# Kernel optimization log

Measured on AMD Instinct MI355X. Metric: run time of the kernel, lower is better.

Reference implementation:

```python
import jax, jax.numpy as jnp
import numpy as np

APPERTURE = 256
Q_SCALE = 0.06


def setup_inputs() -> dict:
    key = jax.random.key(0)
    ks = jax.random.split(key, 5)
    B, N, D_IN, D_OUT = 4, 4096, 1024, 1024
    std = 1.0 / np.sqrt(D_IN)
    x = jax.random.normal(ks[0], (B, N, D_IN), dtype=jnp.float32)
    Wk = jax.random.normal(ks[1], (D_OUT, D_IN), dtype=jnp.float32) * std
    Wq = jax.random.normal(ks[2], (D_OUT, D_IN), dtype=jnp.float32) * std
    Wv = jax.random.normal(ks[3], (D_OUT, D_IN), dtype=jnp.float32) * std
    Wo = jax.random.normal(ks[4], (D_IN, D_OUT), dtype=jnp.float32) * std
    return {"x": x, "Wk": Wk, "Wq": Wq, "Wv": Wv, "Wo": Wo}


def reference(x, Wk, Wq, Wv, Wo):
    # x: [B, N, D_in]; torch Linear(W) computes x @ W.T
    K = jnp.einsum('bnd,od->bno', x, Wk)          # [B, N, D_out]
    Q = jnp.einsum('bnd,od->bno', x, Wq) * Q_SCALE
    V = jnp.einsum('bnd,od->bno', x, Wv)
    logits = jnp.einsum('bno,bmo->bnm', Q, K)      # [B, N, N]
    N = x.shape[1]
    idx = jnp.arange(N)
    # tril(-a) + triu(a) masks |i-j| >= apperture (keep strict band)
    band_mask = jnp.abs(idx[:, None] - idx[None, :]) >= APPERTURE  # [N, N]
    logits = jnp.where(band_mask[None, :, :], -jnp.inf, logits)
    att_weights = jax.nn.softmax(logits, axis=-1)  # [B, N, N]
    # dropout is identity in eval mode
    # y = (V^T @ weights)^T  ->  y[b,n,:] = sum_m att[b,m,n] * V[b,m,:]
    y = jnp.einsum('bmn,bmo->bno', att_weights, V)
    y = jnp.einsum('bno,io->bni', y, Wo)           # [B, N, D_in]
    return (y, att_weights)
```

## Files before the change

### kernel.cpp

```cpp
#include <hip/hip_runtime.h>
#include <stdint.h>

#define SEQ 4096
#define DM  1024
#define NB  4
#define QSCALE 0.06f

typedef __attribute__((ext_vector_type(8))) short short8;
typedef __attribute__((ext_vector_type(4))) float floatx4;

__device__ __forceinline__ unsigned short f2bf(float f) {
  union { float f; unsigned int u; } v; v.f = f;
  unsigned int u = v.u;
  u += 0x7FFFu + ((u >> 16) & 1u);
  return (unsigned short)(u >> 16);
}

__device__ __forceinline__ void async16(const void* g, void* l) {
  __builtin_amdgcn_global_load_lds(
      (const __attribute__((address_space(1))) void*)g,
      (__attribute__((address_space(3))) void*)l, 16, 0, 0);
}

__global__ void cvt_all(const float* __restrict__ x, const float* __restrict__ wk,
                        const float* __restrict__ wq, const float* __restrict__ wv,
                        const float* __restrict__ wo, unsigned short* __restrict__ xb,
                        unsigned short* __restrict__ wb) {
  int blk = blockIdx.x;
  const float* src;
  unsigned short* dst;
  int i;
  if (blk < 8192) {
    src = x; dst = xb; i = (blk * 256 + threadIdx.x) * 8;
  } else {
    int w = blk - 8192;
    int sel = w >> 9;
    src = sel == 0 ? wk : sel == 1 ? wq : sel == 2 ? wv : wo;
    dst = wb + sel * 1048576;
    i = ((w & 511) * 256 + threadIdx.x) * 8;
  }
  const float4* p = (const float4*)(src + i);
  float4 a = p[0], b = p[1];
  short8 o;
  o[0] = (short)f2bf(a.x); o[1] = (short)f2bf(a.y);
  o[2] = (short)f2bf(a.z); o[3] = (short)f2bf(a.w);
  o[4] = (short)f2bf(b.x); o[5] = (short)f2bf(b.y);
  o[6] = (short)f2bf(b.z); o[7] = (short)f2bf(b.w);
  *(short8*)(dst + i) = o;
}

template <bool OUT_BF16, int MT, int NT, bool DUAL>
__global__ __launch_bounds__(512, 2) void gemm256(
    const unsigned short* __restrict__ A, const unsigned short* __restrict__ W,
    void* __restrict__ C0, void* __restrict__ C1, float a0, float a1, long ldc) {
  __shared__ __align__(16) unsigned short lds[4 * 16384];
  const int K = 1024;
  const int NKT = 32;
  int tid = threadIdx.x;
  int lane = tid & 63;
  int wid = tid >> 6;
  int wr = wid >> 2, wc = wid & 3;

  const int CPX = (MT * NT) >> 3;
  int bid = blockIdx.x;
  int raw = (bid & 7) * CPX + (bid >> 3);
  int bx = raw % MT;
  int by = raw / MT;
  long brow = (long)bx * 256;
  long bcol = (long)by * 256;

  floatx4 acc[8][4];
#pragma unroll
  for (int i = 0; i < 8; i++)
#pragma unroll
    for (int j = 0; j < 4; j++) acc[i][j] = (floatx4){0.f, 0.f, 0.f, 0.f};

  const unsigned short* Ag = A + (brow + (tid >> 2)) * K + (tid & 3) * 8;
  const unsigned short* Wg = W + (bcol + (tid >> 2)) * K + (tid & 3) * 8;
  unsigned short* ldsW = lds + wid * 512;

  int aRd = (wr * 128 + (lane & 15)) * 32 + (lane >> 4) * 8;
  int bRd = (wc * 64 + (lane & 15)) * 32 + (lane >> 4) * 8;

#pragma unroll
  for (int tt = 0; tt < 3; tt++) {
    unsigned short* d = ldsW + tt * 16384;
    const unsigned short* a = Ag + tt * 32;
    const unsigned short* w = Wg + tt * 32;
    async16(a, d);
    async16(a + 128 * K, d + 4096);
    async16(w, d + 8192);
    async16(w + 128 * K, d + 12288);
  }
  asm volatile("s_waitcnt vmcnt(8)" ::: "memory");
  __builtin_amdgcn_s_barrier();

  for (int t = 0; t < NKT; ++t) {
    const unsigned short* bufA = lds + (t & 3) * 16384;
    const unsigned short* bufB = bufA + 8192;
    short8 a0f[4], b0f[4], a1f[4];
#pragma unroll
    for (int mt = 0; mt < 4; mt++)
      a0f[mt] = *(const short8*)(bufA + aRd + mt * 512);
#pragma unroll
    for (int nt = 0; nt < 4; nt++)
      b0f[nt] = *(const short8*)(bufB + bRd + nt * 512);
    if (t + 3 < NKT) {
      unsigned short* d = ldsW + ((t + 3) & 3) * 16384;
      const unsigned short* a = Ag + (t + 3) * 32;
      async16(a, d);
      async16(a + 128 * K, d + 4096);
    }
    __builtin_amdgcn_s_barrier();
    __builtin_amdgcn_s_setprio(1);
#pragma unroll
    for (int mt = 0; mt < 4; mt++)
#pragma unroll
      for (int nt = 0; nt < 4; nt++)
        acc[mt][nt] = __builtin_amdgcn_mfma_f32_16x16x32_bf16(
            a0f[mt], b0f[nt], acc[mt][nt], 0, 0, 0);
    __builtin_amdgcn_s_setprio(0);
    __builtin_amdgcn_s_barrier();
#pragma unroll
    for (int mt = 0; mt < 4; mt++)
      a1f[mt] = *(const short8*)(bufA + aRd + 2048 + mt * 512);
    if (t + 3 < NKT) {
      unsigned short* d = ldsW + ((t + 3) & 3) * 16384;
      const unsigned short* w = Wg + (t + 3) * 32;
      async16(w, d + 8192);
      async16(w + 128 * K, d + 12288);
    }
    __builtin_amdgcn_s_barrier();
    __builtin_amdgcn_s_setprio(1);
#pragma unroll
    for (int mt = 0; mt < 4; mt++)
#pragma unroll
      for (int nt = 0; nt < 4; nt++)
        acc[4 + mt][nt] = __builtin_amdgcn_mfma_f32_16x16x32_bf16(
            a1f[mt], b0f[nt], acc[4 + mt][nt], 0, 0, 0);
    __builtin_amdgcn_s_setprio(0);
    if (t < NKT - 3)
      asm volatile("s_waitcnt vmcnt(8)" ::: "memory");
    else if (t == NKT - 3)
      asm volatile("s_waitcnt vmcnt(4)" ::: "memory");
    else
      asm volatile("s_waitcnt vmcnt(0)" ::: "memory");
    __builtin_amdgcn_s_barrier();
  }

  void* Cp;
  float alpha;
  long cc;
  if (DUAL && by >= NT / 2) {
    Cp = C1; alpha = a1; cc = bcol - (long)(NT / 2) * 256;
  } else {
    Cp = C0; alpha = a0; cc = bcol;
  }
  long crow = brow + wr * 128 + (lane >> 4) * 4;
  long ccol = cc + wc * 64 + (lane & 15);
#pragma unroll
  for (int mt = 0; mt < 8; mt++)
#pragma unroll
    for (int nt = 0; nt < 4; nt++)
#pragma unroll
      for (int r = 0; r < 4; r++) {
        float v = acc[mt][nt][r] * alpha;
        long idx = (crow + mt * 16 + r) * ldc + ccol + nt * 16;
        if (OUT_BF16)
          ((unsigned short*)Cp)[idx] = f2bf(v);
        else
          ((float*)Cp)[idx] = v;
      }
}

__global__ __launch_bounds__(512, 2) void logits256(
    const unsigned short* __restrict__ Qb, const unsigned short* __restrict__ Kb,
    float* __restrict__ att) {
  int b = blockIdx.z;
  int n0 = blockIdx.x * 256;
  int m0 = n0 + ((int)blockIdx.y - 1) * 256;
  if (m0 < 0 || m0 >= SEQ) return;
  __shared__ __align__(16) unsigned short lds[4 * 16384];
  const int K = 1024;
  const int NKT = 32;
  int tid = threadIdx.x;
  int lane = tid & 63;
  int wid = tid >> 6;
  int wr = wid >> 2, wc = wid & 3;

  floatx4 acc[8][4];
#pragma unroll
  for (int i = 0; i < 8; i++)
#pragma unroll
    for (int j = 0; j < 4; j++) acc[i][j] = (floatx4){0.f, 0.f, 0.f, 0.f};

  const unsigned short* Ag =
      Qb + ((long)b * SEQ + n0 + (tid >> 2)) * K + (tid & 3) * 8;
  const unsigned short* Wg =
      Kb + ((long)b * SEQ + m0 + (tid >> 2)) * K + (tid & 3) * 8;
  unsigned short* ldsW = lds + wid * 512;

  int aRd = (wr * 128 + (lane & 15)) * 32 + (lane >> 4) * 8;
  int bRd = (wc * 64 + (lane & 15)) * 32 + (lane >> 4) * 8;

#pragma unroll
  for (int tt = 0; tt < 3; tt++) {
    unsigned short* d = ldsW + tt * 16384;
    const unsigned short* a = Ag + tt * 32;
    const unsigned short* w = Wg + tt * 32;
    async16(a, d);
    async16(a + 128 * K, d + 4096);
    async16(w, d + 8192);
    async16(w + 128 * K, d + 12288);
  }
  asm volatile("s_waitcnt vmcnt(8)" ::: "memory");
  __builtin_amdgcn_s_barrier();

  for (int t = 0; t < NKT; ++t) {
    const unsigned short* bufA = lds + (t & 3) * 16384;
    const unsigned short* bufB = bufA + 8192;
    short8 a0f[4], b0f[4], a1f[4];
#pragma unroll
    for (int mt = 0; mt < 4; mt++)
      a0f[mt] = *(const short8*)(bufA + aRd + mt * 512);
#pragma unroll
    for (int nt = 0; nt < 4; nt++)
      b0f[nt] = *(const short8*)(bufB + bRd + nt * 512);
    if (t + 3 < NKT) {
      unsigned short* d = ldsW + ((t + 3) & 3) * 16384;
      const unsigned short* a = Ag + (t + 3) * 32;
      async16(a, d);
      async16(a + 128 * K, d + 4096);
    }
    __builtin_amdgcn_s_barrier();
    __builtin_amdgcn_s_setprio(1);
#pragma unroll
    for (int mt = 0; mt < 4; mt++)
#pragma unroll
      for (int nt = 0; nt < 4; nt++)
        acc[mt][nt] = __builtin_amdgcn_mfma_f32_16x16x32_bf16(
            a0f[mt], b0f[nt], acc[mt][nt], 0, 0, 0);
    __builtin_amdgcn_s_setprio(0);
    __builtin_amdgcn_s_barrier();
#pragma unroll
    for (int mt = 0; mt < 4; mt++)
      a1f[mt] = *(const short8*)(bufA + aRd + 2048 + mt * 512);
    if (t + 3 < NKT) {
      unsigned short* d = ldsW + ((t + 3) & 3) * 16384;
      const unsigned short* w = Wg + (t + 3) * 32;
      async16(w, d + 8192);
      async16(w + 128 * K, d + 12288);
    }
    __builtin_amdgcn_s_barrier();
    __builtin_amdgcn_s_setprio(1);
#pragma unroll
    for (int mt = 0; mt < 4; mt++)
#pragma unroll
      for (int nt = 0; nt < 4; nt++)
        acc[4 + mt][nt] = __builtin_amdgcn_mfma_f32_16x16x32_bf16(
            a1f[mt], b0f[nt], acc[4 + mt][nt], 0, 0, 0);
    __builtin_amdgcn_s_setprio(0);
    if (t < NKT - 3)
      asm volatile("s_waitcnt vmcnt(8)" ::: "memory");
    else if (t == NKT - 3)
      asm volatile("s_waitcnt vmcnt(4)" ::: "memory");
    else
      asm volatile("s_waitcnt vmcnt(0)" ::: "memory");
    __builtin_amdgcn_s_barrier();
  }

  float* attB = att + (long)b * SEQ * SEQ;
  int crow = n0 + wr * 128 + (lane >> 4) * 4;
  int ccol = m0 + wc * 64 + (lane & 15);
#pragma unroll
  for (int mt = 0; mt < 8; mt++)
#pragma unroll
    for (int nt = 0; nt < 4; nt++)
#pragma unroll
      for (int r = 0; r < 4; r++) {
        int row = crow + mt * 16 + r;
        int col = ccol + nt * 16;
        int d = row - col;
        if (d < 256 && d > -256)
          attB[(long)row * SEQ + col] = acc[mt][nt][r];
      }
}

__global__ __launch_bounds__(256) void softmax_band(
    float* __restrict__ att, unsigned short* __restrict__ attT2) {
  __shared__ float e_lds[16 * 545];
  __shared__ float inv_s[16];
  int blk = blockIdx.x;
  int b = blk >> 8;
  int r0 = (blk & 255) * 16;
  int tid = threadIdx.x;
  int row = tid >> 4;
  int t16 = tid & 15;
  int i = r0 + row;
  int jbase = r0 - 272;
  float* arow = att + ((long)b * SEQ + i) * (long)SEQ;

  float raw[34];
  float m = -1e30f;
#pragma unroll
  for (int s = 0; s < 34; s++) {
    int jj = s * 16 + t16;
    int j = jbase + jj;
    bool ok = (j >= 0) && (j < SEQ) && (j >= i - 255) && (j <= i + 255);
    float v = ok ? arow[j] : -1e30f;
    raw[s] = v;
    m = fmaxf(m, v);
  }
#pragma unroll
  for (int off = 8; off; off >>= 1) m = fmaxf(m, __shfl_xor(m, off, 16));

  float sum = 0.f;
#pragma unroll
  for (int s = 0; s < 34; s++) {
    int jj = s * 16 + t16;
    float e = (raw[s] > -1e29f) ? __expf(raw[s] - m) : 0.f;
    e_lds[row * 545 + jj] = e;
    sum += e;
  }
#pragma unroll
  for (int off = 8; off; off >>= 1) sum += __shfl_xor(sum, off, 16);
  float invr = 1.0f / sum;
  if (t16 == 0) inv_s[row] = invr;
  __syncthreads();

  for (int s = 0; s < 64; s++) {
    int j0 = (s * 16 + t16) * 4;
    float4 w;
    float* wp = (float*)&w;
#pragma unroll
    for (int k = 0; k < 4; k++) {
      int j = j0 + k;
      bool ok = (j >= i - 255) && (j <= i + 255);
      int jj = j - jbase;
      jj = jj < 0 ? 0 : (jj > 543 ? 543 : jj);
      wp[k] = ok ? e_lds[row * 545 + jj] * invr : 0.f;
    }
    *(float4*)(arow + j0) = w;
  }

  int nn = tid >> 4;
  int mi16 = tid & 15;
  int i2 = r0 + mi16;
  float inv2 = inv_s[mi16];
  int Bc = r0 & ~255;
  for (int s = 0; s < 48; s++) {
    int n = Bc - 256 + s * 16 + nn;
    if (n < 0 || n >= SEQ) continue;
    int mi = i2 - (n & ~255) + 256;
    bool ok = (n >= i2 - 255) && (n <= i2 + 255);
    int jj = n - jbase;
    jj = jj < 0 ? 0 : (jj > 544 ? 544 : jj);
    float val = ok ? e_lds[mi16 * 545 + jj] * inv2 : 0.f;
    attT2[(((long)b * 16 + (n >> 8)) * 256 + (n & 255)) * 768 + mi] = f2bf(val);
  }
}

__global__ __launch_bounds__(512, 2) void attv256(
    const unsigned short* __restrict__ attT2, const unsigned short* __restrict__ Vt,
    unsigned short* __restrict__ yb) {
  __shared__ __align__(16) unsigned short lds[4 * 16384];
  const int KA = 768;
  const int NKT = 24;
  int b = blockIdx.z;
  int nb2 = blockIdx.x;
  int o0 = blockIdx.y * 256;
  int N0 = nb2 * 256;
  int tid = threadIdx.x;
  int lane = tid & 63;
  int wid = tid >> 6;
  int wr = wid >> 2, wc = wid & 3;

  floatx4 acc[8][4];
#pragma unroll
  for (int i = 0; i < 8; i++)
#pragma unroll
    for (int j = 0; j < 4; j++) acc[i][j] = (floatx4){0.f, 0.f, 0.f, 0.f};

  const unsigned short* Abase = attT2 + ((long)(b * 16 + nb2) * 256) * KA;
  const unsigned short* Ag = Abase + (long)(tid >> 2) * KA + (tid & 3) * 8;
  const unsigned short* Vg =
      Vt + (long)(o0 + (tid >> 2)) * (NB * SEQ) + (tid & 3) * 8;
  unsigned short* ldsW = lds + wid * 512;

  int aRd = (wr * 128 + (lane & 15)) * 32 + (lane >> 4) * 8;
  int bRd = (wc * 64 + (lane & 15)) * 32 + (lane >> 4) * 8;

  auto boff = [&](int t) {
    int mg = N0 - 256 + t * 32;
    int mc = mg < 0 ? 0 : (mg > SEQ - 32 ? SEQ - 32 : mg);
    return (long)b * SEQ + mc;
  };

#pragma unroll
  for (int tt = 0; tt < 3; tt++) {
    unsigned short* d = ldsW + tt * 16384;
    async16(Ag + tt * 32, d);
    async16(Ag + 128 * KA + tt * 32, d + 4096);
    long bo = boff(tt);
    async16(Vg + bo, d + 8192);
    async16(Vg + 128L * (NB * SEQ) + bo, d + 12288);
  }
  asm volatile("s_waitcnt vmcnt(8)" ::: "memory");
  __builtin_amdgcn_s_barrier();

  for (int t = 0; t < NKT; ++t) {
    int mg = N0 - 256 + t * 32;
    bool live = (mg > -32) && (mg < SEQ);
    const unsigned short* bufA = lds + (t & 3) * 16384;
    const unsigned short* bufB = bufA + 8192;
    short8 a0f[4], b0f[4], a1f[4];
#pragma unroll
    for (int mt = 0; mt < 4; mt++)
      a0f[mt] = *(const short8*)(bufA + aRd + mt * 512);
#pragma unroll
    for (int nt = 0; nt < 4; nt++)
      b0f[nt] = *(const short8*)(bufB + bRd + nt * 512);
    if (t + 3 < NKT) {
      unsigned short* d = ldsW + ((t + 3) & 3) * 16384;
      async16(Ag + (t + 3) * 32, d);
      async16(Ag + 128 * KA + (t + 3) * 32, d + 4096);
    }
    __builtin_amdgcn_s_barrier();
    if (live) {
      __builtin_amdgcn_s_setprio(1);
#pragma unroll
      for (int mt = 0; mt < 4; mt++)
#pragma unroll
        for (int nt = 0; nt < 4; nt++)
          acc[mt][nt] = __builtin_amdgcn_mfma_f32_16x16x32_bf16(
              a0f[mt], b0f[nt], acc[mt][nt], 0, 0, 0);
      __builtin_amdgcn_s_setprio(0);
    }
    __builtin_amdgcn_s_barrier();
#pragma unroll
    for (int mt = 0; mt < 4; mt++)
      a1f[mt] = *(const short8*)(bufA + aRd + 2048 + mt * 512);
    if (t + 3 < NKT) {
      unsigned short* d = ldsW + ((t + 3) & 3) * 16384;
      long bo = boff(t + 3);
      async16(Vg + bo, d + 8192);
      async16(Vg + 128L * (NB * SEQ) + bo, d + 12288);
    }
    __builtin_amdgcn_s_barrier();
    if (live) {
      __builtin_amdgcn_s_setprio(1);
#pragma unroll
      for (int mt = 0; mt < 4; mt++)
#pragma unroll
        for (int nt = 0; nt < 4; nt++)
          acc[4 + mt][nt] = __builtin_amdgcn_mfma_f32_16x16x32_bf16(
              a1f[mt], b0f[nt], acc[4 + mt][nt], 0, 0, 0);
      __builtin_amdgcn_s_setprio(0);
    }
    if (t < NKT - 3)
      asm volatile("s_waitcnt vmcnt(8)" ::: "memory");
    else if (t == NKT - 3)
      asm volatile("s_waitcnt vmcnt(4)" ::: "memory");
    else
      asm volatile("s_waitcnt vmcnt(0)" ::: "memory");
    __builtin_amdgcn_s_barrier();
  }

  long crow = (long)b * SEQ + N0 + wr * 128 + (lane >> 4) * 4;
  int ccol = o0 + wc * 64 + (lane & 15);
#pragma unroll
  for (int mt = 0; mt < 8; mt++)
#pragma unroll
    for (int nt = 0; nt < 4; nt++)
#pragma unroll
      for (int r = 0; r < 4; r++)
        yb[(crow + mt * 16 + r) * DM + ccol + nt * 16] = f2bf(acc[mt][nt][r]);
}

extern "C" void kernel_launch(void* const* d_in, const int* in_sizes, int n_in,
                              void* d_out, int out_size, void* d_ws, size_t ws_size,
                              hipStream_t stream) {
  const float* x  = (const float*)d_in[0];
  const float* Wk = (const float*)d_in[1];
  const float* Wq = (const float*)d_in[2];
  const float* Wv = (const float*)d_in[3];
  const float* Wo = (const float*)d_in[4];
  float* outY = (float*)d_out;
  float* outAtt = outY + (long)NB * SEQ * DM;

  char* ws = (char*)d_ws;
  unsigned short* xb  = (unsigned short*)(ws + 0);
  unsigned short* Kb  = (unsigned short*)(ws + 33554432);
  unsigned short* Qb  = (unsigned short*)(ws + 67108864);
  unsigned short* Vt  = (unsigned short*)(ws + 100663296);
  unsigned short* Wkb = (unsigned short*)(ws + 134217728);
  unsigned short* Wvb = Wkb + 2097152;
  unsigned short* Wob = Wvb + 1048576;
  unsigned short* attT2 = Kb;
  unsigned short* yb = xb;

  cvt_all<<<10240, 256, 0, stream>>>(x, Wk, Wq, Wv, Wo, xb, Wkb);

  gemm256<true, 64, 8, true><<<512, 512, 0, stream>>>(
      xb, Wkb, Kb, Qb, 1.0f, QSCALE, 1024);
  gemm256<true, 4, 64, false><<<256, 512, 0, stream>>>(
      Wvb, xb, Vt, nullptr, 1.0f, 1.0f, NB * SEQ);

  logits256<<<dim3(16, 3, NB), 512, 0, stream>>>(Qb, Kb, outAtt);
  softmax_band<<<1024, 256, 0, stream>>>(outAtt, attT2);
  attv256<<<dim3(16, 4, NB), 512, 0, stream>>>(attT2, Vt, yb);
  gemm256<false, 64, 4, false><<<256, 512, 0, stream>>>(
      yb, Wob, outY, nullptr, 1.0f, 1.0f, 1024);
}
```

Before: 640.0 us.

## Merge K/Q/V projection launches and drop mid-iteration barriers in GEMM loops

The K/Q and V projection GEMMs now run in one launch by dispatching on block index, so their 768 blocks share one grid instead of two back-to-back launches. In the GEMM, logits and attv main loops, all LDS fragment reads for a k-step are done up front and all four async prefetches are issued together. Both MFMA halves then run with no intra-iteration barriers, leaving one barrier per step. The change cuts synchronisation and launch overhead, but raises register pressure from holding more fragments and loses the interleaving of prefetch with compute.

```diff
diff --git a/kernel.cpp b/kernel.cpp
--- a/kernel.cpp
+++ b/kernel.cpp
@@ -50,10 +50,10 @@
 }
 
 template <bool OUT_BF16, int MT, int NT, bool DUAL>
-__global__ __launch_bounds__(512, 2) void gemm256(
+__device__ __forceinline__ void gemm_body(
+    unsigned short* lds, int bid,
     const unsigned short* __restrict__ A, const unsigned short* __restrict__ W,
     void* __restrict__ C0, void* __restrict__ C1, float a0, float a1, long ldc) {
-  __shared__ __align__(16) unsigned short lds[4 * 16384];
   const int K = 1024;
   const int NKT = 32;
   int tid = threadIdx.x;
@@ -62,7 +62,6 @@
   int wr = wid >> 2, wc = wid & 3;
 
   const int CPX = (MT * NT) >> 3;
-  int bid = blockIdx.x;
   int raw = (bid & 7) * CPX + (bid >> 3);
   int bx = raw % MT;
   int by = raw / MT;
@@ -105,13 +104,18 @@
 #pragma unroll
     for (int nt = 0; nt < 4; nt++)
       b0f[nt] = *(const short8*)(bufB + bRd + nt * 512);
+#pragma unroll
+    for (int mt = 0; mt < 4; mt++)
+      a1f[mt] = *(const short8*)(bufA + aRd + 2048 + mt * 512);
     if (t + 3 < NKT) {
       unsigned short* d = ldsW + ((t + 3) & 3) * 16384;
       const unsigned short* a = Ag + (t + 3) * 32;
+      const unsigned short* w = Wg + (t + 3) * 32;
       async16(a, d);
       async16(a + 128 * K, d + 4096);
+      async16(w, d + 8192);
+      async16(w + 128 * K, d + 12288);
     }
-    __builtin_amdgcn_s_barrier();
     __builtin_amdgcn_s_setprio(1);
 #pragma unroll
     for (int mt = 0; mt < 4; mt++)
@@ -119,19 +123,6 @@
       for (int nt = 0; nt < 4; nt++)
         acc[mt][nt] = __builtin_amdgcn_mfma_f32_16x16x32_bf16(
             a0f[mt], b0f[nt], acc[mt][nt], 0, 0, 0);
-    __builtin_amdgcn_s_setprio(0);
-    __builtin_amdgcn_s_barrier();
-#pragma unroll
-    for (int mt = 0; mt < 4; mt++)
-      a1f[mt] = *(const short8*)(bufA + aRd + 2048 + mt * 512);
-    if (t + 3 < NKT) {
-      unsigned short* d = ldsW + ((t + 3) & 3) * 16384;
-      const unsigned short* w = Wg + (t + 3) * 32;
-      async16(w, d + 8192);
-      async16(w + 128 * K, d + 12288);
-    }
-    __builtin_amdgcn_s_barrier();
-    __builtin_amdgcn_s_setprio(1);
 #pragma unroll
     for (int mt = 0; mt < 4; mt++)
 #pragma unroll
@@ -171,6 +162,27 @@
         else
           ((float*)Cp)[idx] = v;
       }
+}
+
+__global__ __launch_bounds__(512, 2) void proj_fused(
+    const unsigned short* __restrict__ xb, const unsigned short* __restrict__ Wkb,
+    const unsigned short* __restrict__ Wvb, unsigned short* __restrict__ Kb,
+    unsigned short* __restrict__ Qb, unsigned short* __restrict__ Vt) {
+  __shared__ __align__(16) unsigned short lds[4 * 16384];
+  if (blockIdx.x < 512)
+    gemm_body<true, 64, 8, true>(lds, blockIdx.x, xb, Wkb, Kb, Qb, 1.0f, QSCALE,
+                                 1024);
+  else
+    gemm_body<true, 4, 64, false>(lds, blockIdx.x - 512, Wvb, xb, Vt, nullptr,
+                                  1.0f, 1.0f, (long)NB * SEQ);
+}
+
+__global__ __launch_bounds__(512, 2) void gemm_wo(
+    const unsigned short* __restrict__ yb, const unsigned short* __restrict__ Wob,
+    float* __restrict__ outY) {
+  __shared__ __align__(16) unsigned short lds[4 * 16384];
+  gemm_body<false, 64, 4, false>(lds, blockIdx.x, yb, Wob, outY, nullptr, 1.0f,
+                                 1.0f, 1024);
 }
 
 __global__ __launch_bounds__(512, 2) void logits256(
@@ -226,13 +238,18 @@
 #pragma unroll
     for (int nt = 0; nt < 4; nt++)
       b0f[nt] = *(const short8*)(bufB + bRd + nt * 512);
+#pragma unroll
+    for (int mt = 0; mt < 4; mt++)
+      a1f[mt] = *(const short8*)(bufA + aRd + 2048 + mt * 512);
     if (t + 3 < NKT) {
       unsigned short* d = ldsW + ((t + 3) & 3) * 16384;
       const unsigned short* a = Ag + (t + 3) * 32;
+      const unsigned short* w = Wg + (t + 3) * 32;
       async16(a, d);
       async16(a + 128 * K, d + 4096);
+      async16(w, d + 8192);
+      async16(w + 128 * K, d + 12288);
     }
-    __builtin_amdgcn_s_barrier();
     __builtin_amdgcn_s_setprio(1);
 #pragma unroll
     for (int mt = 0; mt < 4; mt++)
@@ -240,19 +257,6 @@
       for (int nt = 0; nt < 4; nt++)
         acc[mt][nt] = __builtin_amdgcn_mfma_f32_16x16x32_bf16(
             a0f[mt], b0f[nt], acc[mt][nt], 0, 0, 0);
-    __builtin_amdgcn_s_setprio(0);
-    __builtin_amdgcn_s_barrier();
-#pragma unroll
-    for (int mt = 0; mt < 4; mt++)
-      a1f[mt] = *(const short8*)(bufA + aRd + 2048 + mt * 512);
-    if (t + 3 < NKT) {
-      unsigned short* d = ldsW + ((t + 3) & 3) * 16384;
-      const unsigned short* w = Wg + (t + 3) * 32;
-      async16(w, d + 8192);
-      async16(w + 128 * K, d + 12288);
-    }
-    __builtin_amdgcn_s_barrier();
-    __builtin_amdgcn_s_setprio(1);
 #pragma unroll
     for (int mt = 0; mt < 4; mt++)
 #pragma unroll
@@ -420,35 +424,25 @@
 #pragma unroll
     for (int nt = 0; nt < 4; nt++)
       b0f[nt] = *(const short8*)(bufB + bRd + nt * 512);
-    if (t + 3 < NKT) {
-      unsigned short* d = ldsW + ((t + 3) & 3) * 16384;
-      async16(Ag + (t + 3) * 32, d);
-      async16(Ag + 128 * KA + (t + 3) * 32, d + 4096);
-    }
-    __builtin_amdgcn_s_barrier();
-    if (live) {
-      __builtin_amdgcn_s_setprio(1);
-#pragma unroll
-      for (int mt = 0; mt < 4; mt++)
-#pragma unroll
-        for (int nt = 0; nt < 4; nt++)
-          acc[mt][nt] = __builtin_amdgcn_mfma_f32_16x16x32_bf16(
-              a0f[mt], b0f[nt], acc[mt][nt], 0, 0, 0);
-      __builtin_amdgcn_s_setprio(0);
-    }
-    __builtin_amdgcn_s_barrier();
 #pragma unroll
     for (int mt = 0; mt < 4; mt++)
       a1f[mt] = *(const short8*)(bufA + aRd + 2048 + mt * 512);
     if (t + 3 < NKT) {
       unsigned short* d = ldsW + ((t + 3) & 3) * 16384;
       long bo = boff(t + 3);
+      async16(Ag + (t + 3) * 32, d);
+      async16(Ag + 128 * KA + (t + 3) * 32, d + 4096);
       async16(Vg + bo, d + 8192);
       async16(Vg + 128L * (NB * SEQ) + bo, d + 12288);
     }
-    __builtin_amdgcn_s_barrier();
     if (live) {
       __builtin_amdgcn_s_setprio(1);
+#pragma unroll
+      for (int mt = 0; mt < 4; mt++)
+#pragma unroll
+        for (int nt = 0; nt < 4; nt++)
+          acc[mt][nt] = __builtin_amdgcn_mfma_f32_16x16x32_bf16(
+              a0f[mt], b0f[nt], acc[mt][nt], 0, 0, 0);
 #pragma unroll
       for (int mt = 0; mt < 4; mt++)
 #pragma unroll
@@ -500,15 +494,9 @@
   unsigned short* yb = xb;
 
   cvt_all<<<10240, 256, 0, stream>>>(x, Wk, Wq, Wv, Wo, xb, Wkb);
-
-  gemm256<true, 64, 8, true><<<512, 512, 0, stream>>>(
-      xb, Wkb, Kb, Qb, 1.0f, QSCALE, 1024);
-  gemm256<true, 4, 64, false><<<256, 512, 0, stream>>>(
-      Wvb, xb, Vt, nullptr, 1.0f, 1.0f, NB * SEQ);
-
+  proj_fused<<<768, 512, 0, stream>>>(xb, Wkb, Wvb, Kb, Qb, Vt);
   logits256<<<dim3(16, 3, NB), 512, 0, stream>>>(Qb, Kb, outAtt);
   softmax_band<<<1024, 256, 0, stream>>>(outAtt, attT2);
   attv256<<<dim3(16, 4, NB), 512, 0, stream>>>(attT2, Vt, yb);
-  gemm256<false, 64, 4, false><<<256, 512, 0, stream>>>(
-      yb, Wob, outY, nullptr, 1.0f, 1.0f, 1024);
-}
+  gemm_wo<<<256, 512, 0, stream>>>(yb, Wob, outY);
+}
```

Result: faster. 620.9 us (-3.0%).
